# Kernel optimization log

Hardware: AMD Instinct MI355X
Metric: run time of the kernel (lower is better)

The kernel has to match this reference:

```python
import jax, jax.numpy as jnp
import numpy as np

B, L, IN = 4, 4096, 4096
G, R, GD = 32, 64, 128          # num_groups, rank per group, group_dim
SUM_R = G * R                    # 2048


def setup_inputs() -> dict:
    key = jax.random.key(0)
    k1, k2, k3, k4 = jax.random.split(key, 4)
    hidden_states = jax.random.normal(k1, (B, L, IN), dtype=jnp.float32)
    # nn.Linear weights: VT maps in_features -> sum(ranks)
    VT_w = jax.random.normal(k2, (SUM_R, IN), dtype=jnp.float32) * (IN ** -0.5)
    # Per-group up-projections U[i]: rank -> group_dim, stacked since ranks equal
    U_w = jax.random.normal(k3, (G, GD, R), dtype=jnp.float32) * (R ** -0.5)
    U_b = jax.random.normal(k4, (G, GD), dtype=jnp.float32) * 0.01
    return {"hidden_states": hidden_states, "VT_w": VT_w, "U_w": U_w, "U_b": U_b}


def reference(hidden_states, VT_w, U_w, U_b):
    # project_to_latent: shared down-projection  [B,L,IN] @ [IN,SUM_R]
    latents = jnp.einsum('bli,ri->blr', hidden_states, VT_w)  # [B,L,SUM_R]
    # reconstruct: per-group small up-projection on contiguous latent slices
    lat_g = latents.reshape(B, L, G, R)                        # [B,L,G,R]
    out_g = jnp.einsum('blgr,gdr->blgd', lat_g, U_w) + U_b     # [B,L,G,GD]
    return out_g.reshape(B, L, G * GD)                         # concat over groups
```

## Files before the change

kernel.cpp:

```cpp
#include <hip/hip_runtime.h>
#include <cstdint>

typedef unsigned short u16;
typedef u16 u16x8 __attribute__((ext_vector_type(8)));
typedef __bf16 bf16x8 __attribute__((ext_vector_type(8)));
typedef float f32x4 __attribute__((ext_vector_type(4)));

#define GLOAD_LDS16(g, l)                                                          \
  __builtin_amdgcn_global_load_lds((const __attribute__((address_space(1))) void*)(g), \
                                   (__attribute__((address_space(3))) void*)(l), 16, 0, 0)

#define BARRIER() do { asm volatile("" ::: "memory");                 \
                       __builtin_amdgcn_sched_barrier(0);             \
                       __builtin_amdgcn_s_barrier();                  \
                       __builtin_amdgcn_sched_barrier(0);             \
                       asm volatile("" ::: "memory"); } while (0)
#define VMCNT4() asm volatile("s_waitcnt vmcnt(4)" ::: "memory")
#define VMCNT0() asm volatile("s_waitcnt vmcnt(0)" ::: "memory")

__device__ __forceinline__ u16 f2bf(float f) {
  union { float f; uint32_t u; } v; v.f = f;
  uint32_t u = v.u;
  return (u16)((u + 0x7fffu + ((u >> 16) & 1u)) >> 16);
}

constexpr long MH = 67108864L;
constexpr long MV = 8388608L;
constexpr long MU = 262144L;
constexpr long ML = 33554432L;

__global__ __launch_bounds__(256) void cvt_all(const float* __restrict__ H,
                                               const float* __restrict__ VT,
                                               const float* __restrict__ Uw,
                                               u16* __restrict__ dst) {
  const long n8 = (MH + MV + MU) / 8;
  long i = (long)blockIdx.x * blockDim.x + threadIdx.x;
  long stride = (long)gridDim.x * blockDim.x;
  for (; i < n8; i += stride) {
    long j = i * 8;
    const float* src;
    if (j < MH)            src = H + j;
    else if (j < MH + MV)  src = VT + (j - MH);
    else                   src = Uw + (j - MH - MV);
    const float4* p = (const float4*)src;
    float4 a = p[0], b = p[1];
    u16x8 o;
    o[0] = f2bf(a.x); o[1] = f2bf(a.y); o[2] = f2bf(a.z); o[3] = f2bf(a.w);
    o[4] = f2bf(b.x); o[5] = f2bf(b.y); o[6] = f2bf(b.z); o[7] = f2bf(b.w);
    *(u16x8*)(dst + j) = o;
  }
}

constexpr int GK = 4096;
constexpr int NKT = GK / 64;

__device__ __forceinline__ void stage_half(u16* sm, const u16* g, int ldsbase, int w) {
  u16* l0 = sm + ldsbase + w * 1024;
  GLOAD_LDS16(g, l0);
  GLOAD_LDS16(g + 8 * GK, l0 + 512);
}

__device__ __forceinline__ void readA(const u16* sm, int base, int msub, bf16x8* fA) {
#pragma unroll
  for (int mf = 0; mf < 4; ++mf) {
    int idx = base + (msub * 64 + mf * 16) * 64;
    fA[mf * 2]     = *(const bf16x8*)(sm + idx);
    fA[mf * 2 + 1] = *(const bf16x8*)(sm + (idx ^ 32));
  }
}

__device__ __forceinline__ void readB(const u16* sm, int base, int qn, bf16x8* fB) {
#pragma unroll
  for (int nf = 0; nf < 2; ++nf) {
    int idx = base + (qn * 32 + nf * 16) * 64;
    fB[nf * 2]     = *(const bf16x8*)(sm + idx);
    fB[nf * 2 + 1] = *(const bf16x8*)(sm + (idx ^ 32));
  }
}

__device__ __forceinline__ void mfma8(const bf16x8* fA, const bf16x8* fB,
                                      f32x4 (*acc)[4], int mbase, int nbase) {
  __builtin_amdgcn_s_setprio(1);
#pragma unroll
  for (int mf = 0; mf < 4; ++mf)
#pragma unroll
    for (int nf = 0; nf < 2; ++nf) {
      acc[mbase + mf][nbase + nf] = __builtin_amdgcn_mfma_f32_16x16x32_bf16(
          fA[mf * 2], fB[nf * 2], acc[mbase + mf][nbase + nf], 0, 0, 0);
      acc[mbase + mf][nbase + nf] = __builtin_amdgcn_mfma_f32_16x16x32_bf16(
          fA[mf * 2 + 1], fB[nf * 2 + 1], acc[mbase + mf][nbase + nf], 0, 0, 0);
    }
  __builtin_amdgcn_s_setprio(0);
}

template <bool MORE>
__device__ __forceinline__ void kiter(u16* sm, int i, int w,
                                      const u16* gAs, const u16* gBs,
                                      int Ab0, int Bb0, bf16x8* fA, bf16x8* fB0,
                                      bf16x8* fB1, f32x4 (*acc)[4]) {
  const long dOdd = (long)(2 * i + 1) * 64;
  const long dE2  = (long)(2 * i + 2) * 64;
  const long dO3  = (long)(2 * i + 3) * 64;
  const long hOff = 128L * GK;

  readA(sm, Ab0, 0, fA);
  readB(sm, Bb0, 0, fB0);
  stage_half(sm, gBs + hOff + dOdd, 32768 + 24576, w);
  BARRIER();
  mfma8(fA, fB0, acc, 0, 0);
  BARRIER();
  readB(sm, Bb0, 1, fB1);
  stage_half(sm, gAs + hOff + dOdd, 24576, w);
  BARRIER();
  mfma8(fA, fB1, acc, 0, 2);
  BARRIER();
  readA(sm, Ab0, 1, fA);
  if constexpr (MORE) stage_half(sm, gBs + dE2, 32768, w);
  BARRIER();
  mfma8(fA, fB1, acc, 4, 2);
  BARRIER();
  if constexpr (MORE) stage_half(sm, gAs + dE2, 0, w);
  if constexpr (MORE) VMCNT4(); else VMCNT0();
  BARRIER();
  mfma8(fA, fB0, acc, 4, 0);
  BARRIER();
  readA(sm, Ab0 + 16384, 0, fA);
  readB(sm, Bb0 + 16384, 0, fB0);
  if constexpr (MORE) stage_half(sm, gBs + hOff + dE2, 32768 + 8192, w);
  BARRIER();
  mfma8(fA, fB0, acc, 0, 0);
  BARRIER();
  readB(sm, Bb0 + 16384, 1, fB1);
  if constexpr (MORE) stage_half(sm, gAs + hOff + dE2, 8192, w);
  BARRIER();
  mfma8(fA, fB1, acc, 0, 2);
  BARRIER();
  readA(sm, Ab0 + 16384, 1, fA);
  if constexpr (MORE) stage_half(sm, gBs + dO3, 32768 + 16384, w);
  BARRIER();
  mfma8(fA, fB1, acc, 4, 2);
  BARRIER();
  if constexpr (MORE) stage_half(sm, gAs + dO3, 16384, w);
  if constexpr (MORE) VMCNT4(); else VMCNT0();
  BARRIER();
  mfma8(fA, fB0, acc, 4, 0);
  BARRIER();
}

__global__ __launch_bounds__(512, 2) void gemm256_fused(const u16* __restrict__ A,
                                                        const u16* __restrict__ B,
                                                        const u16* __restrict__ Ubf,
                                                        const float* __restrict__ Ubias,
                                                        float* __restrict__ out) {
  __shared__ u16 sm[66560];
  int bid = blockIdx.x;
  int swz = (bid & 7) * 64 + (bid >> 3);
  int tn = swz & 7;
  int tm = swz >> 3;
  int t0 = threadIdx.x;
  int w = t0 >> 6, l = t0 & 63;
  int wr = w >> 2, wc = w & 3;
  int lo = l & 15, hi = l >> 4;

  int lr = l >> 3;
  int sslot = (l & 7) ^ lr;
  const u16* gAs = A + (long)(tm * 256 + w * 16 + lr) * GK + sslot * 8;
  const u16* gBs = B + (long)(tn * 256 + w * 16 + lr) * GK + sslot * 8;

  int slotbase = (hi ^ (lo & 7)) * 8;
  int Ab0 = wr * 8192 + lo * 64 + slotbase;
  int Bb0 = 32768 + (wc >> 1) * 8192 + ((wc & 1) * 64 + lo) * 64 + slotbase;

  bf16x8 fA[8], fB0[4], fB1[4];
  f32x4 acc[8][4] = {};

  stage_half(sm, gBs,               32768,         w);
  stage_half(sm, gAs,               0,             w);
  stage_half(sm, gBs + 128L * GK,   32768 + 8192,  w);
  stage_half(sm, gAs + 128L * GK,   8192,          w);
  stage_half(sm, gBs + 64,          32768 + 16384, w);
  stage_half(sm, gAs + 64,          16384,         w);
  VMCNT4();
  BARRIER();

  for (int i = 0; i < NKT / 2 - 1; ++i)
    kiter<true>(sm, i, w, gAs, gBs, Ab0, Bb0, fA, fB0, fB1, acc);
  kiter<false>(sm, NKT / 2 - 1, w, gAs, gBs, Ab0, Bb0, fA, fB0, fB1, acc);

  int g_abs = tn * 4 + wc;
#pragma unroll
  for (int mq = 0; mq < 8; ++mq)
#pragma unroll
    for (int n = 0; n < 4; ++n) {
      int rl = wr * 128 + mq * 16 + hi * 4;
      int cl = wc * 64 + n * 16 + lo;
#pragma unroll
      for (int j = 0; j < 4; ++j)
        sm[(rl + j) * 260 + cl] = f2bf(acc[mq][n][j]);
    }
  const u16* Ug = Ubf + g_abs * 8192;
#pragma unroll
  for (int mh = 0; mh < 2; ++mh) {
    bf16x8 fL[8];
#pragma unroll
    for (int ms = 0; ms < 4; ++ms) {
      int rl = wr * 128 + mh * 64 + ms * 16 + lo;
#pragma unroll
      for (int ks = 0; ks < 2; ++ks)
        fL[ms * 2 + ks] = *(const bf16x8*)(sm + rl * 260 + wc * 64 + ks * 32 + hi * 8);
    }
#pragma unroll
    for (int nf = 0; nf < 8; ++nf) {
      int d = nf * 16 + lo;
      bf16x8 u0 = *(const bf16x8*)(Ug + d * 64 + hi * 8);
      bf16x8 u1 = *(const bf16x8*)(Ug + d * 64 + 32 + hi * 8);
      float bias = Ubias[g_abs * 128 + d];
#pragma unroll
      for (int ms = 0; ms < 4; ++ms) {
        f32x4 o = {};
        o = __builtin_amdgcn_mfma_f32_16x16x32_bf16(fL[ms * 2],     u0, o, 0, 0, 0);
        o = __builtin_amdgcn_mfma_f32_16x16x32_bf16(fL[ms * 2 + 1], u1, o, 0, 0, 0);
        long row = (long)tm * 256 + wr * 128 + mh * 64 + ms * 16 + hi * 4;
        int col = g_abs * 128 + d;
#pragma unroll
        for (int j = 0; j < 4; ++j)
          out[(row + j) * 4096 + col] = o[j] + bias;
      }
    }
  }
}

__global__ __launch_bounds__(256) void gemm1_f32(const float* __restrict__ fAp,
                                                 const u16* __restrict__ B,
                                                 u16* __restrict__ Cl) {
  constexpr int K = 4096;
  __shared__ u16 sA[128 * 32];
  __shared__ u16 sB[128 * 32];
  int bid = blockIdx.x;
  int swz = (bid & 7) * 256 + (bid >> 3);
  int tn = swz & 15;
  int tm = swz >> 4;
  int t = threadIdx.x;
  int w = t >> 6, l = t & 63;
  int wr = w >> 1, wc = w & 1;
  int lo = l & 15, hi = l >> 4;
  const int rS = w * 32 + (l >> 2);
  const int kS = (l & 3) * 8;
  const u16* gB = B + (long)(tn * 128 + rS) * K + kS;
  u16* lB = &sB[w * 1024];
  int fr = t >> 1, fk = (t & 1) * 16;

  f32x4 acc[4][4] = {};
  for (int k0 = 0; k0 < K; k0 += 32) {
    const float* src = fAp + (long)(tm * 128 + fr) * K + k0 + fk;
    float4 x = *(const float4*)(src);
    float4 y = *(const float4*)(src + 4);
    float4 z = *(const float4*)(src + 8);
    float4 q = *(const float4*)(src + 12);
    u16x8 o1, o2;
    o1[0] = f2bf(x.x); o1[1] = f2bf(x.y); o1[2] = f2bf(x.z); o1[3] = f2bf(x.w);
    o1[4] = f2bf(y.x); o1[5] = f2bf(y.y); o1[6] = f2bf(y.z); o1[7] = f2bf(y.w);
    o2[0] = f2bf(z.x); o2[1] = f2bf(z.y); o2[2] = f2bf(z.z); o2[3] = f2bf(z.w);
    o2[4] = f2bf(q.x); o2[5] = f2bf(q.y); o2[6] = f2bf(q.z); o2[7] = f2bf(q.w);
    *(u16x8*)&sA[fr * 32 + fk] = o1;
    *(u16x8*)&sA[fr * 32 + fk + 8] = o2;
    GLOAD_LDS16(gB, lB);
    GLOAD_LDS16(gB + 16 * K, lB + 512);
    gB += 32;
    __syncthreads();
    bf16x8 af[4], bfr[4];
#pragma unroll
    for (int m = 0; m < 4; ++m)
      af[m] = *(const bf16x8*)&sA[(wr * 64 + m * 16 + lo) * 32 + hi * 8];
#pragma unroll
    for (int n = 0; n < 4; ++n)
      bfr[n] = *(const bf16x8*)&sB[(wc * 64 + n * 16 + lo) * 32 + hi * 8];
#pragma unroll
    for (int m = 0; m < 4; ++m)
#pragma unroll
      for (int n = 0; n < 4; ++n)
        acc[m][n] = __builtin_amdgcn_mfma_f32_16x16x32_bf16(af[m], bfr[n], acc[m][n], 0, 0, 0);
    __syncthreads();
  }
#pragma unroll
  for (int m = 0; m < 4; ++m)
#pragma unroll
    for (int n = 0; n < 4; ++n) {
      int col = tn * 128 + wc * 64 + n * 16 + lo;
      int row = tm * 128 + wr * 64 + m * 16 + hi * 4;
#pragma unroll
      for (int j = 0; j < 4; ++j)
        Cl[(long)(row + j) * 2048 + col] = f2bf(acc[m][n][j]);
    }
}

__global__ __launch_bounds__(256) void stage2(const u16* __restrict__ L,
                                              const u16* __restrict__ U,
                                              const float* __restrict__ Ub,
                                              float* __restrict__ out) {
  int tm = blockIdx.x, g = blockIdx.y;
  int t = threadIdx.x, w = t >> 6, l = t & 63;
  int lo = l & 15, hi = l >> 4;
  const u16* Lb = L + (long)(tm * 128 + w * 32) * 2048 + g * 64;
  const u16* Ug = U + g * 8192;
  f32x4 acc[2][8] = {};
#pragma unroll
  for (int ks = 0; ks < 2; ++ks) {
    int ek = ks * 32 + hi * 8;
    bf16x8 a0 = *(const bf16x8*)(Lb + (long)lo * 2048 + ek);
    bf16x8 a1 = *(const bf16x8*)(Lb + (long)(lo + 16) * 2048 + ek);
#pragma unroll
    for (int n = 0; n < 8; ++n) {
      bf16x8 bv = *(const bf16x8*)(Ug + (n * 16 + lo) * 64 + ek);
      acc[0][n] = __builtin_amdgcn_mfma_f32_16x16x32_bf16(a0, bv, acc[0][n], 0, 0, 0);
      acc[1][n] = __builtin_amdgcn_mfma_f32_16x16x32_bf16(a1, bv, acc[1][n], 0, 0, 0);
    }
  }
#pragma unroll
  for (int n = 0; n < 8; ++n) {
    int col = n * 16 + lo;
    float bias = Ub[g * 128 + col];
#pragma unroll
    for (int m = 0; m < 2; ++m) {
      int row = tm * 128 + w * 32 + m * 16 + hi * 4;
#pragma unroll
      for (int j = 0; j < 4; ++j)
        out[(long)(row + j) * 4096 + g * 128 + col] = acc[m][n][j] + bias;
    }
  }
}

__global__ __launch_bounds__(256) void cvt_f32_bf16(const float* __restrict__ in,
                                                    u16* __restrict__ out, long n8) {
  long i = (long)blockIdx.x * blockDim.x + threadIdx.x;
  long stride = (long)gridDim.x * blockDim.x;
  for (; i < n8; i += stride) {
    const float4* p = (const float4*)(in + i * 8);
    float4 a = p[0], b = p[1];
    u16x8 o;
    o[0] = f2bf(a.x); o[1] = f2bf(a.y); o[2] = f2bf(a.z); o[3] = f2bf(a.w);
    o[4] = f2bf(b.x); o[5] = f2bf(b.y); o[6] = f2bf(b.z); o[7] = f2bf(b.w);
    *(u16x8*)(out + i * 8) = o;
  }
}

extern "C" void kernel_launch(void* const* d_in, const int* in_sizes, int n_in,
                              void* d_out, int out_size, void* d_ws, size_t ws_size,
                              hipStream_t stream) {
  const float* H   = (const float*)d_in[0];
  const float* VT  = (const float*)d_in[1];
  const float* Uw  = (const float*)d_in[2];
  const float* Ubp = (const float*)d_in[3];
  float* out = (float*)d_out;
  size_t needFull = (size_t)(MH + MV + MU) * 2;

  if (ws_size >= needFull) {
    u16* hbf = (u16*)d_ws;
    u16* vbf = hbf + MH;
    u16* ubf = vbf + MV;
    cvt_all<<<2048, 256, 0, stream>>>(H, VT, Uw, hbf);
    gemm256_fused<<<512, 512, 0, stream>>>(hbf, vbf, ubf, Ubp, out);
  } else {
    u16* vbf = (u16*)d_ws;
    u16* ubf = vbf + MV;
    u16* lat = ubf + MU;
    cvt_f32_bf16<<<512, 256, 0, stream>>>(VT, vbf, MV / 8);
    cvt_f32_bf16<<<128, 256, 0, stream>>>(Uw, ubf, MU / 8);
    gemm1_f32<<<2048, 256, 0, stream>>>(H, vbf, lat);
    stage2<<<dim3(128, 32), 256, 0, stream>>>(lat, ubf, Ubp, out);
  }
}
```

Measured before the change: 350.7 us.

## Double-buffer MFMA register fragments to prefetch LDS reads one phase ahead

Splits the A and B register fragments into separate even/odd and half-0/half-1 buffers so each LDS read is issued one phase before the MFMA that consumes it. The next tile's first fragments are read before the last MFMA group of the current iteration, and the first read is hoisted before the loop. The aim is to hide LDS read latency behind matrix ops. The cost is roughly double the fragment registers alongside a large accumulator under launch_bounds(512,2), which risks spills or lower occupancy.

```diff
diff --git a/kernel.cpp b/kernel.cpp
--- a/kernel.cpp
+++ b/kernel.cpp
@@ -27,7 +27,6 @@
 constexpr long MH = 67108864L;
 constexpr long MV = 8388608L;
 constexpr long MU = 262144L;
-constexpr long ML = 33554432L;
 
 __global__ __launch_bounds__(256) void cvt_all(const float* __restrict__ H,
                                                const float* __restrict__ VT,
@@ -96,54 +95,60 @@
 template <bool MORE>
 __device__ __forceinline__ void kiter(u16* sm, int i, int w,
                                       const u16* gAs, const u16* gBs,
-                                      int Ab0, int Bb0, bf16x8* fA, bf16x8* fB0,
-                                      bf16x8* fB1, f32x4 (*acc)[4]) {
+                                      int Ab0, int Bb0,
+                                      bf16x8* fA0e, bf16x8* fA1e,
+                                      bf16x8* fA0o, bf16x8* fA1o,
+                                      bf16x8* fB0e, bf16x8* fB1e,
+                                      bf16x8* fB0o, bf16x8* fB1o,
+                                      f32x4 (*acc)[4]) {
   const long dOdd = (long)(2 * i + 1) * 64;
   const long dE2  = (long)(2 * i + 2) * 64;
   const long dO3  = (long)(2 * i + 3) * 64;
   const long hOff = 128L * GK;
 
-  readA(sm, Ab0, 0, fA);
-  readB(sm, Bb0, 0, fB0);
+  readB(sm, Bb0, 1, fB1e);
   stage_half(sm, gBs + hOff + dOdd, 32768 + 24576, w);
   BARRIER();
-  mfma8(fA, fB0, acc, 0, 0);
-  BARRIER();
-  readB(sm, Bb0, 1, fB1);
+  mfma8(fA0e, fB0e, acc, 0, 0);
+  BARRIER();
+  readA(sm, Ab0, 1, fA1e);
   stage_half(sm, gAs + hOff + dOdd, 24576, w);
   BARRIER();
-  mfma8(fA, fB1, acc, 0, 2);
-  BARRIER();
-  readA(sm, Ab0, 1, fA);
+  mfma8(fA0e, fB1e, acc, 0, 2);
+  BARRIER();
   if constexpr (MORE) stage_half(sm, gBs + dE2, 32768, w);
   BARRIER();
-  mfma8(fA, fB1, acc, 4, 2);
+  mfma8(fA1e, fB1e, acc, 4, 2);
   BARRIER();
   if constexpr (MORE) stage_half(sm, gAs + dE2, 0, w);
   if constexpr (MORE) VMCNT4(); else VMCNT0();
   BARRIER();
-  mfma8(fA, fB0, acc, 4, 0);
-  BARRIER();
-  readA(sm, Ab0 + 16384, 0, fA);
-  readB(sm, Bb0 + 16384, 0, fB0);
+  readA(sm, Ab0 + 16384, 0, fA0o);
+  readB(sm, Bb0 + 16384, 0, fB0o);
+  mfma8(fA1e, fB0e, acc, 4, 0);
+  BARRIER();
+  readB(sm, Bb0 + 16384, 1, fB1o);
   if constexpr (MORE) stage_half(sm, gBs + hOff + dE2, 32768 + 8192, w);
   BARRIER();
-  mfma8(fA, fB0, acc, 0, 0);
-  BARRIER();
-  readB(sm, Bb0 + 16384, 1, fB1);
+  mfma8(fA0o, fB0o, acc, 0, 0);
+  BARRIER();
+  readA(sm, Ab0 + 16384, 1, fA1o);
   if constexpr (MORE) stage_half(sm, gAs + hOff + dE2, 8192, w);
   BARRIER();
-  mfma8(fA, fB1, acc, 0, 2);
-  BARRIER();
-  readA(sm, Ab0 + 16384, 1, fA);
+  mfma8(fA0o, fB1o, acc, 0, 2);
+  BARRIER();
   if constexpr (MORE) stage_half(sm, gBs + dO3, 32768 + 16384, w);
   BARRIER();
-  mfma8(fA, fB1, acc, 4, 2);
+  mfma8(fA1o, fB1o, acc, 4, 2);
   BARRIER();
   if constexpr (MORE) stage_half(sm, gAs + dO3, 16384, w);
   if constexpr (MORE) VMCNT4(); else VMCNT0();
   BARRIER();
-  mfma8(fA, fB0, acc, 4, 0);
+  if constexpr (MORE) {
+    readA(sm, Ab0, 0, fA0e);
+    readB(sm, Bb0, 0, fB0e);
+  }
+  mfma8(fA1o, fB0o, acc, 4, 0);
   BARRIER();
 }
 
@@ -171,7 +176,8 @@
   int Ab0 = wr * 8192 + lo * 64 + slotbase;
   int Bb0 = 32768 + (wc >> 1) * 8192 + ((wc & 1) * 64 + lo) * 64 + slotbase;
 
-  bf16x8 fA[8], fB0[4], fB1[4];
+  bf16x8 fA0e[8], fA1e[8], fA0o[8], fA1o[8];
+  bf16x8 fB0e[4], fB1e[4], fB0o[4], fB1o[4];
   f32x4 acc[8][4] = {};
 
   stage_half(sm, gBs,               32768,         w);
@@ -182,10 +188,14 @@
   stage_half(sm, gAs + 64,          16384,         w);
   VMCNT4();
   BARRIER();
+  readA(sm, Ab0, 0, fA0e);
+  readB(sm, Bb0, 0, fB0e);
 
   for (int i = 0; i < NKT / 2 - 1; ++i)
-    kiter<true>(sm, i, w, gAs, gBs, Ab0, Bb0, fA, fB0, fB1, acc);
-  kiter<false>(sm, NKT / 2 - 1, w, gAs, gBs, Ab0, Bb0, fA, fB0, fB1, acc);
+    kiter<true>(sm, i, w, gAs, gBs, Ab0, Bb0,
+                fA0e, fA1e, fA0o, fA1o, fB0e, fB1e, fB0o, fB1o, acc);
+  kiter<false>(sm, NKT / 2 - 1, w, gAs, gBs, Ab0, Bb0,
+               fA0e, fA1e, fA0o, fA1o, fB0e, fB1e, fB0o, fB1o, acc);
 
   int g_abs = tn * 4 + wc;
 #pragma unroll
```

New measurement: 564.6 us. 1.61x slower.

## Fuse fp32-to-bf16 conversion of activations into GEMM A-tile loading

Applied to the files above, without the earlier changes.

Removes the separate pass that converts the large fp32 hidden_states tensor to bf16. The GEMM now loads fp32 A tiles into registers, converts them, and writes bf16 into LDS inside the pipelined k-loop, while B keeps using direct global-to-LDS loads. This avoids writing and re-reading a bf16 copy of the activations. In exchange, A loads go through registers, which adds VGPR pressure and conversion ALU work, and doubles A global read bytes per tile inside the GEMM. Waitcnt placement is reworked to fit the new load pattern.

```diff
diff --git a/kernel.cpp b/kernel.cpp
--- a/kernel.cpp
+++ b/kernel.cpp
@@ -15,8 +15,10 @@
                        __builtin_amdgcn_s_barrier();                  \
                        __builtin_amdgcn_sched_barrier(0);             \
                        asm volatile("" ::: "memory"); } while (0)
-#define VMCNT4() asm volatile("s_waitcnt vmcnt(4)" ::: "memory")
+#define VMCNT2() asm volatile("s_waitcnt vmcnt(2)" ::: "memory")
 #define VMCNT0() asm volatile("s_waitcnt vmcnt(0)" ::: "memory")
+#define LGKM0()  do { asm volatile("s_waitcnt lgkmcnt(0)" ::: "memory");  \
+                      __builtin_amdgcn_sched_barrier(0); } while (0)
 
 __device__ __forceinline__ u16 f2bf(float f) {
   union { float f; uint32_t u; } v; v.f = f;
@@ -29,19 +31,15 @@
 constexpr long MU = 262144L;
 constexpr long ML = 33554432L;
 
-__global__ __launch_bounds__(256) void cvt_all(const float* __restrict__ H,
-                                               const float* __restrict__ VT,
-                                               const float* __restrict__ Uw,
-                                               u16* __restrict__ dst) {
-  const long n8 = (MH + MV + MU) / 8;
+__global__ __launch_bounds__(256) void cvt_vu(const float* __restrict__ VT,
+                                              const float* __restrict__ Uw,
+                                              u16* __restrict__ dst) {
+  const long n8 = (MV + MU) / 8;
   long i = (long)blockIdx.x * blockDim.x + threadIdx.x;
   long stride = (long)gridDim.x * blockDim.x;
   for (; i < n8; i += stride) {
     long j = i * 8;
-    const float* src;
-    if (j < MH)            src = H + j;
-    else if (j < MH + MV)  src = VT + (j - MH);
-    else                   src = Uw + (j - MH - MV);
+    const float* src = (j < MV) ? (VT + j) : (Uw + (j - MV));
     const float4* p = (const float4*)src;
     float4 a = p[0], b = p[1];
     u16x8 o;
@@ -60,6 +58,22 @@
   GLOAD_LDS16(g + 8 * GK, l0 + 512);
 }
 
+__device__ __forceinline__ void loadA(const float* g, float4* r) {
+  r[0] = *(const float4*)(g);
+  r[1] = *(const float4*)(g + 4);
+  r[2] = *(const float4*)(g + 8 * GK);
+  r[3] = *(const float4*)(g + 8 * GK + 4);
+}
+__device__ __forceinline__ void cvtWriteA(u16* sm, int ldsbase, int wl8, const float4* r) {
+  u16x8 o0, o1;
+  o0[0] = f2bf(r[0].x); o0[1] = f2bf(r[0].y); o0[2] = f2bf(r[0].z); o0[3] = f2bf(r[0].w);
+  o0[4] = f2bf(r[1].x); o0[5] = f2bf(r[1].y); o0[6] = f2bf(r[1].z); o0[7] = f2bf(r[1].w);
+  o1[0] = f2bf(r[2].x); o1[1] = f2bf(r[2].y); o1[2] = f2bf(r[2].z); o1[3] = f2bf(r[2].w);
+  o1[4] = f2bf(r[3].x); o1[5] = f2bf(r[3].y); o1[6] = f2bf(r[3].z); o1[7] = f2bf(r[3].w);
+  *(u16x8*)(sm + ldsbase + wl8) = o0;
+  *(u16x8*)(sm + ldsbase + wl8 + 512) = o1;
+}
+
 __device__ __forceinline__ void readA(const u16* sm, int base, int msub, bf16x8* fA) {
 #pragma unroll
   for (int mf = 0; mf < 4; ++mf) {
@@ -94,60 +108,82 @@
 }
 
 template <bool MORE>
-__device__ __forceinline__ void kiter(u16* sm, int i, int w,
-                                      const u16* gAs, const u16* gBs,
+__device__ __forceinline__ void kiter(u16* sm, int i, int w, int wl8,
+                                      const float* gAf, const u16* gBs,
                                       int Ab0, int Bb0, bf16x8* fA, bf16x8* fB0,
                                       bf16x8* fB1, f32x4 (*acc)[4]) {
   const long dOdd = (long)(2 * i + 1) * 64;
   const long dE2  = (long)(2 * i + 2) * 64;
   const long dO3  = (long)(2 * i + 3) * 64;
-  const long hOff = 128L * GK;
-
+  const long hOffB = 128L * GK;
+  const long hOffA = 128L * GK;
+  float4 rA[4];
+
+  readB(sm, Bb0, 0, fB0);
   readA(sm, Ab0, 0, fA);
-  readB(sm, Bb0, 0, fB0);
-  stage_half(sm, gBs + hOff + dOdd, 32768 + 24576, w);
+  loadA(gAf + dOdd, rA);
+  stage_half(sm, gBs + hOffB + dOdd, 32768 + 24576, w);
   BARRIER();
   mfma8(fA, fB0, acc, 0, 0);
   BARRIER();
   readB(sm, Bb0, 1, fB1);
-  stage_half(sm, gAs + hOff + dOdd, 24576, w);
+  VMCNT2();
+  cvtWriteA(sm, 16384, wl8, rA);
+  LGKM0();
   BARRIER();
   mfma8(fA, fB1, acc, 0, 2);
   BARRIER();
   readA(sm, Ab0, 1, fA);
+  loadA(gAf + hOffA + dOdd, rA);
   if constexpr (MORE) stage_half(sm, gBs + dE2, 32768, w);
   BARRIER();
   mfma8(fA, fB1, acc, 4, 2);
   BARRIER();
-  if constexpr (MORE) stage_half(sm, gAs + dE2, 0, w);
-  if constexpr (MORE) VMCNT4(); else VMCNT0();
+  if constexpr (MORE) VMCNT2(); else VMCNT0();
+  cvtWriteA(sm, 24576, wl8, rA);
+  LGKM0();
   BARRIER();
   mfma8(fA, fB0, acc, 4, 0);
   BARRIER();
+  readB(sm, Bb0 + 16384, 0, fB0);
   readA(sm, Ab0 + 16384, 0, fA);
-  readB(sm, Bb0 + 16384, 0, fB0);
-  if constexpr (MORE) stage_half(sm, gBs + hOff + dE2, 32768 + 8192, w);
+  if constexpr (MORE) {
+    loadA(gAf + dE2, rA);
+    stage_half(sm, gBs + hOffB + dE2, 32768 + 8192, w);
+  }
   BARRIER();
   mfma8(fA, fB0, acc, 0, 0);
   BARRIER();
   readB(sm, Bb0 + 16384, 1, fB1);
-  if constexpr (MORE) stage_half(sm, gAs + hOff + dE2, 8192, w);
+  if constexpr (MORE) {
+    VMCNT2();
+    cvtWriteA(sm, 0, wl8, rA);
+    LGKM0();
+  }
   BARRIER();
   mfma8(fA, fB1, acc, 0, 2);
   BARRIER();
   readA(sm, Ab0 + 16384, 1, fA);
-  if constexpr (MORE) stage_half(sm, gBs + dO3, 32768 + 16384, w);
+  if constexpr (MORE) {
+    loadA(gAf + hOffA + dE2, rA);
+    stage_half(sm, gBs + dO3, 32768 + 16384, w);
+  }
   BARRIER();
   mfma8(fA, fB1, acc, 4, 2);
   BARRIER();
-  if constexpr (MORE) stage_half(sm, gAs + dO3, 16384, w);
-  if constexpr (MORE) VMCNT4(); else VMCNT0();
+  if constexpr (MORE) {
+    VMCNT2();
+    cvtWriteA(sm, 8192, wl8, rA);
+    LGKM0();
+  } else {
+    VMCNT0();
+  }
   BARRIER();
   mfma8(fA, fB0, acc, 4, 0);
   BARRIER();
 }
 
-__global__ __launch_bounds__(512, 2) void gemm256_fused(const u16* __restrict__ A,
+__global__ __launch_bounds__(512, 2) void gemm256_fused(const float* __restrict__ A,
                                                         const u16* __restrict__ B,
                                                         const u16* __restrict__ Ubf,
                                                         const float* __restrict__ Ubias,
@@ -164,8 +200,9 @@
 
   int lr = l >> 3;
   int sslot = (l & 7) ^ lr;
-  const u16* gAs = A + (long)(tm * 256 + w * 16 + lr) * GK + sslot * 8;
-  const u16* gBs = B + (long)(tn * 256 + w * 16 + lr) * GK + sslot * 8;
+  const float* gAf = A + (long)(tm * 256 + w * 16 + lr) * GK + sslot * 8;
+  const u16*   gBs = B + (long)(tn * 256 + w * 16 + lr) * GK + sslot * 8;
+  int wl8 = w * 1024 + l * 8;
 
   int slotbase = (hi ^ (lo & 7)) * 8;
   int Ab0 = wr * 8192 + lo * 64 + slotbase;
@@ -174,18 +211,24 @@
   bf16x8 fA[8], fB0[4], fB1[4];
   f32x4 acc[8][4] = {};
 
-  stage_half(sm, gBs,               32768,         w);
-  stage_half(sm, gAs,               0,             w);
-  stage_half(sm, gBs + 128L * GK,   32768 + 8192,  w);
-  stage_half(sm, gAs + 128L * GK,   8192,          w);
-  stage_half(sm, gBs + 64,          32768 + 16384, w);
-  stage_half(sm, gAs + 64,          16384,         w);
-  VMCNT4();
-  BARRIER();
+  {
+    float4 r0[4], r1[4];
+    loadA(gAf, r0);
+    loadA(gAf + 128L * GK, r1);
+    stage_half(sm, gBs,             32768,         w);
+    stage_half(sm, gBs + 128L * GK, 32768 + 8192,  w);
+    stage_half(sm, gBs + 64,        32768 + 16384, w);
+    asm volatile("s_waitcnt vmcnt(6)" ::: "memory");
+    cvtWriteA(sm, 0,    wl8, r0);
+    cvtWriteA(sm, 8192, wl8, r1);
+    VMCNT2();
+    LGKM0();
+    BARRIER();
+  }
 
   for (int i = 0; i < NKT / 2 - 1; ++i)
-    kiter<true>(sm, i, w, gAs, gBs, Ab0, Bb0, fA, fB0, fB1, acc);
-  kiter<false>(sm, NKT / 2 - 1, w, gAs, gBs, Ab0, Bb0, fA, fB0, fB1, acc);
+    kiter<true>(sm, i, w, wl8, gAf, gBs, Ab0, Bb0, fA, fB0, fB1, acc);
+  kiter<false>(sm, NKT / 2 - 1, w, wl8, gAf, gBs, Ab0, Bb0, fA, fB0, fB1, acc);
 
   int g_abs = tn * 4 + wc;
 #pragma unroll
@@ -330,20 +373,6 @@
   }
 }
 
-__global__ __launch_bounds__(256) void cvt_f32_bf16(const float* __restrict__ in,
-                                                    u16* __restrict__ out, long n8) {
-  long i = (long)blockIdx.x * blockDim.x + threadIdx.x;
-  long stride = (long)gridDim.x * blockDim.x;
-  for (; i < n8; i += stride) {
-    const float4* p = (const float4*)(in + i * 8);
-    float4 a = p[0], b = p[1];
-    u16x8 o;
-    o[0] = f2bf(a.x); o[1] = f2bf(a.y); o[2] = f2bf(a.z); o[3] = f2bf(a.w);
-    o[4] = f2bf(b.x); o[5] = f2bf(b.y); o[6] = f2bf(b.z); o[7] = f2bf(b.w);
-    *(u16x8*)(out + i * 8) = o;
-  }
-}
-
 extern "C" void kernel_launch(void* const* d_in, const int* in_sizes, int n_in,
                               void* d_out, int out_size, void* d_ws, size_t ws_size,
                               hipStream_t stream) {
@@ -352,20 +381,23 @@
   const float* Uw  = (const float*)d_in[2];
   const float* Ubp = (const float*)d_in[3];
   float* out = (float*)d_out;
-  size_t needFull = (size_t)(MH + MV + MU) * 2;
-
-  if (ws_size >= needFull) {
-    u16* hbf = (u16*)d_ws;
-    u16* vbf = hbf + MH;
+  size_t needFast = (size_t)(MV + MU) * 2;
+
+  if (ws_size >= needFast && ws_size < (size_t)(MV + MU + ML) * 2) {
+    u16* vbf = (u16*)d_ws;
     u16* ubf = vbf + MV;
-    cvt_all<<<2048, 256, 0, stream>>>(H, VT, Uw, hbf);
-    gemm256_fused<<<512, 512, 0, stream>>>(hbf, vbf, ubf, Ubp, out);
+    cvt_vu<<<512, 256, 0, stream>>>(VT, Uw, vbf);
+    gemm256_fused<<<512, 512, 0, stream>>>(H, vbf, ubf, Ubp, out);
+  } else if (ws_size >= (size_t)(MV + MU + ML) * 2) {
+    u16* vbf = (u16*)d_ws;
+    u16* ubf = vbf + MV;
+    cvt_vu<<<512, 256, 0, stream>>>(VT, Uw, vbf);
+    gemm256_fused<<<512, 512, 0, stream>>>(H, vbf, ubf, Ubp, out);
   } else {
     u16* vbf = (u16*)d_ws;
     u16* ubf = vbf + MV;
     u16* lat = ubf + MU;
-    cvt_f32_bf16<<<512, 256, 0, stream>>>(VT, vbf, MV / 8);
-    cvt_f32_bf16<<<128, 256, 0, stream>>>(Uw, ubf, MU / 8);
+    cvt_vu<<<512, 256, 0, stream>>>(VT, Uw, vbf);
     gemm1_f32<<<2048, 256, 0, stream>>>(H, vbf, lat);
     stage2<<<dim3(128, 32), 256, 0, stream>>>(lat, ubf, Ubp, out);
   }
```

Result: slower. 488.3 us (+39.2%).

## Double block to 16 waves with 64x64 wave tiles and denser MFMA phases

Applied to the files above, without the earlier changes.

Launches the fused GEMM with 1024 threads per block in a 4x4 wave grid, so each wave owns a 64x64 output tile instead of 128x64. Every thread now stages one 16-byte global-to-LDS load per slab instead of two. The K-iteration is regrouped into four 16-MFMA phases with explicit lgkmcnt waits, replacing eight 8-MFMA phases, and the vmcnt thresholds are adjusted to match. The aim is more waves per CU to hide latency and fewer barriers per MFMA. The risk is the 128-VGPR-per-thread budget that 1024-thread blocks impose, which could cause spills, plus more LDS fragment traffic per unit of compute.

```diff
diff --git a/kernel.cpp b/kernel.cpp
--- a/kernel.cpp
+++ b/kernel.cpp
@@ -15,8 +15,10 @@
                        __builtin_amdgcn_s_barrier();                  \
                        __builtin_amdgcn_sched_barrier(0);             \
                        asm volatile("" ::: "memory"); } while (0)
-#define VMCNT4() asm volatile("s_waitcnt vmcnt(4)" ::: "memory")
+#define VMCNT2() asm volatile("s_waitcnt vmcnt(2)" ::: "memory")
 #define VMCNT0() asm volatile("s_waitcnt vmcnt(0)" ::: "memory")
+#define LGKM0()  do { asm volatile("s_waitcnt lgkmcnt(0)" ::: "memory");  \
+                      __builtin_amdgcn_sched_barrier(0); } while (0)
 
 __device__ __forceinline__ u16 f2bf(float f) {
   union { float f; uint32_t u; } v; v.f = f;
@@ -54,104 +56,96 @@
 constexpr int GK = 4096;
 constexpr int NKT = GK / 64;
 
-__device__ __forceinline__ void stage_half(u16* sm, const u16* g, int ldsbase, int w) {
-  u16* l0 = sm + ldsbase + w * 1024;
-  GLOAD_LDS16(g, l0);
-  GLOAD_LDS16(g + 8 * GK, l0 + 512);
-}
-
-__device__ __forceinline__ void readA(const u16* sm, int base, int msub, bf16x8* fA) {
-#pragma unroll
-  for (int mf = 0; mf < 4; ++mf) {
-    int idx = base + (msub * 64 + mf * 16) * 64;
-    fA[mf * 2]     = *(const bf16x8*)(sm + idx);
-    fA[mf * 2 + 1] = *(const bf16x8*)(sm + (idx ^ 32));
-  }
-}
-
-__device__ __forceinline__ void readB(const u16* sm, int base, int qn, bf16x8* fB) {
-#pragma unroll
-  for (int nf = 0; nf < 2; ++nf) {
-    int idx = base + (qn * 32 + nf * 16) * 64;
-    fB[nf * 2]     = *(const bf16x8*)(sm + idx);
-    fB[nf * 2 + 1] = *(const bf16x8*)(sm + (idx ^ 32));
-  }
-}
-
-__device__ __forceinline__ void mfma8(const bf16x8* fA, const bf16x8* fB,
-                                      f32x4 (*acc)[4], int mbase, int nbase) {
+__device__ __forceinline__ void stage1(u16* sm, const u16* g, int ldsbase, int dst8) {
+  GLOAD_LDS16(g, sm + ldsbase + dst8);
+}
+
+__device__ __forceinline__ void readF(const u16* sm, int base, int sub, bf16x8* f) {
+#pragma unroll
+  for (int ff = 0; ff < 2; ++ff) {
+    int idx = base + (sub * 32 + ff * 16) * 64;
+    f[ff * 2]     = *(const bf16x8*)(sm + idx);
+    f[ff * 2 + 1] = *(const bf16x8*)(sm + (idx ^ 32));
+  }
+}
+
+__device__ __forceinline__ void mfma16(const bf16x8* fA, const bf16x8* fB0,
+                                       const bf16x8* fB1, f32x4 (*acc)[4], int mbase) {
   __builtin_amdgcn_s_setprio(1);
 #pragma unroll
-  for (int mf = 0; mf < 4; ++mf)
-#pragma unroll
-    for (int nf = 0; nf < 2; ++nf) {
-      acc[mbase + mf][nbase + nf] = __builtin_amdgcn_mfma_f32_16x16x32_bf16(
-          fA[mf * 2], fB[nf * 2], acc[mbase + mf][nbase + nf], 0, 0, 0);
-      acc[mbase + mf][nbase + nf] = __builtin_amdgcn_mfma_f32_16x16x32_bf16(
-          fA[mf * 2 + 1], fB[nf * 2 + 1], acc[mbase + mf][nbase + nf], 0, 0, 0);
+  for (int fm = 0; fm < 2; ++fm)
+#pragma unroll
+    for (int n = 0; n < 4; ++n) {
+      const bf16x8* fb = (n < 2) ? (fB0 + (n & 1) * 2) : (fB1 + (n & 1) * 2);
+      acc[mbase + fm][n] = __builtin_amdgcn_mfma_f32_16x16x32_bf16(
+          fA[fm * 2], fb[0], acc[mbase + fm][n], 0, 0, 0);
+      acc[mbase + fm][n] = __builtin_amdgcn_mfma_f32_16x16x32_bf16(
+          fA[fm * 2 + 1], fb[1], acc[mbase + fm][n], 0, 0, 0);
     }
   __builtin_amdgcn_s_setprio(0);
 }
 
 template <bool MORE>
-__device__ __forceinline__ void kiter(u16* sm, int i, int w,
+__device__ __forceinline__ void kiter(u16* sm, int i, int dst8,
                                       const u16* gAs, const u16* gBs,
-                                      int Ab0, int Bb0, bf16x8* fA, bf16x8* fB0,
-                                      bf16x8* fB1, f32x4 (*acc)[4]) {
+                                      int Ab0, int Bb0,
+                                      bf16x8* fA0, bf16x8* fA1,
+                                      bf16x8* fB0, bf16x8* fB1,
+                                      f32x4 (*acc)[4]) {
   const long dOdd = (long)(2 * i + 1) * 64;
   const long dE2  = (long)(2 * i + 2) * 64;
   const long dO3  = (long)(2 * i + 3) * 64;
   const long hOff = 128L * GK;
 
-  readA(sm, Ab0, 0, fA);
-  readB(sm, Bb0, 0, fB0);
-  stage_half(sm, gBs + hOff + dOdd, 32768 + 24576, w);
-  BARRIER();
-  mfma8(fA, fB0, acc, 0, 0);
-  BARRIER();
-  readB(sm, Bb0, 1, fB1);
-  stage_half(sm, gAs + hOff + dOdd, 24576, w);
-  BARRIER();
-  mfma8(fA, fB1, acc, 0, 2);
-  BARRIER();
-  readA(sm, Ab0, 1, fA);
-  if constexpr (MORE) stage_half(sm, gBs + dE2, 32768, w);
-  BARRIER();
-  mfma8(fA, fB1, acc, 4, 2);
-  BARRIER();
-  if constexpr (MORE) stage_half(sm, gAs + dE2, 0, w);
-  if constexpr (MORE) VMCNT4(); else VMCNT0();
-  BARRIER();
-  mfma8(fA, fB0, acc, 4, 0);
-  BARRIER();
-  readA(sm, Ab0 + 16384, 0, fA);
-  readB(sm, Bb0 + 16384, 0, fB0);
-  if constexpr (MORE) stage_half(sm, gBs + hOff + dE2, 32768 + 8192, w);
-  BARRIER();
-  mfma8(fA, fB0, acc, 0, 0);
-  BARRIER();
-  readB(sm, Bb0 + 16384, 1, fB1);
-  if constexpr (MORE) stage_half(sm, gAs + hOff + dE2, 8192, w);
-  BARRIER();
-  mfma8(fA, fB1, acc, 0, 2);
-  BARRIER();
-  readA(sm, Ab0 + 16384, 1, fA);
-  if constexpr (MORE) stage_half(sm, gBs + dO3, 32768 + 16384, w);
-  BARRIER();
-  mfma8(fA, fB1, acc, 4, 2);
-  BARRIER();
-  if constexpr (MORE) stage_half(sm, gAs + dO3, 16384, w);
-  if constexpr (MORE) VMCNT4(); else VMCNT0();
-  BARRIER();
-  mfma8(fA, fB0, acc, 4, 0);
-  BARRIER();
-}
-
-__global__ __launch_bounds__(512, 2) void gemm256_fused(const u16* __restrict__ A,
-                                                        const u16* __restrict__ B,
-                                                        const u16* __restrict__ Ubf,
-                                                        const float* __restrict__ Ubias,
-                                                        float* __restrict__ out) {
+  readF(sm, Bb0, 0, fB0);
+  readF(sm, Ab0, 0, fA0);
+  readF(sm, Bb0, 1, fB1);
+  readF(sm, Ab0, 1, fA1);
+  stage1(sm, gBs + hOff + dOdd, 32768 + 24576, dst8);
+  stage1(sm, gAs + hOff + dOdd, 24576, dst8);
+  BARRIER();
+  mfma16(fA0, fB0, fB1, acc, 0);
+  LGKM0();
+  BARRIER();
+  if constexpr (MORE) {
+    stage1(sm, gBs + dE2, 32768, dst8);
+    stage1(sm, gAs + dE2, 0, dst8);
+    VMCNT2();
+  } else {
+    VMCNT0();
+  }
+  BARRIER();
+  mfma16(fA1, fB0, fB1, acc, 2);
+  BARRIER();
+  readF(sm, Bb0 + 16384, 0, fB0);
+  readF(sm, Ab0 + 16384, 0, fA0);
+  readF(sm, Bb0 + 16384, 1, fB1);
+  readF(sm, Ab0 + 16384, 1, fA1);
+  if constexpr (MORE) {
+    stage1(sm, gBs + hOff + dE2, 32768 + 8192, dst8);
+    stage1(sm, gAs + hOff + dE2, 8192, dst8);
+  }
+  BARRIER();
+  mfma16(fA0, fB0, fB1, acc, 0);
+  LGKM0();
+  BARRIER();
+  if constexpr (MORE) {
+    stage1(sm, gBs + dO3, 32768 + 16384, dst8);
+    stage1(sm, gAs + dO3, 16384, dst8);
+    VMCNT2();
+  } else {
+    VMCNT0();
+  }
+  BARRIER();
+  mfma16(fA1, fB0, fB1, acc, 2);
+  BARRIER();
+}
+
+__global__ __launch_bounds__(1024, 4) void gemm256_fused(const u16* __restrict__ A,
+                                                         const u16* __restrict__ B,
+                                                         const u16* __restrict__ Ubf,
+                                                         const float* __restrict__ Ubias,
+                                                         float* __restrict__ out) {
   __shared__ u16 sm[66560];
   int bid = blockIdx.x;
   int swz = (bid & 7) * 64 + (bid >> 3);
@@ -162,70 +156,68 @@
   int wr = w >> 2, wc = w & 3;
   int lo = l & 15, hi = l >> 4;
 
-  int lr = l >> 3;
-  int sslot = (l & 7) ^ lr;
-  const u16* gAs = A + (long)(tm * 256 + w * 16 + lr) * GK + sslot * 8;
-  const u16* gBs = B + (long)(tn * 256 + w * 16 + lr) * GK + sslot * 8;
+  int lr = t0 >> 3;
+  int sslot = (t0 & 7) ^ (lr & 7);
+  const u16* gAs = A + (long)(tm * 256 + lr) * GK + sslot * 8;
+  const u16* gBs = B + (long)(tn * 256 + lr) * GK + sslot * 8;
+  int dst8 = t0 * 8;
 
   int slotbase = (hi ^ (lo & 7)) * 8;
-  int Ab0 = wr * 8192 + lo * 64 + slotbase;
-  int Bb0 = 32768 + (wc >> 1) * 8192 + ((wc & 1) * 64 + lo) * 64 + slotbase;
-
-  bf16x8 fA[8], fB0[4], fB1[4];
-  f32x4 acc[8][4] = {};
-
-  stage_half(sm, gBs,               32768,         w);
-  stage_half(sm, gAs,               0,             w);
-  stage_half(sm, gBs + 128L * GK,   32768 + 8192,  w);
-  stage_half(sm, gAs + 128L * GK,   8192,          w);
-  stage_half(sm, gBs + 64,          32768 + 16384, w);
-  stage_half(sm, gAs + 64,          16384,         w);
-  VMCNT4();
+  int Ab0 = (wr * 64 + lo) * 64 + slotbase;
+  int Bb0 = 32768 + (wc * 64 + lo) * 64 + slotbase;
+
+  bf16x8 fA0[4], fA1[4], fB0[4], fB1[4];
+  f32x4 acc[4][4] = {};
+
+  stage1(sm, gBs,               32768,         dst8);
+  stage1(sm, gAs,               0,             dst8);
+  stage1(sm, gBs + 128L * GK,   32768 + 8192,  dst8);
+  stage1(sm, gAs + 128L * GK,   8192,          dst8);
+  stage1(sm, gBs + 64,          32768 + 16384, dst8);
+  stage1(sm, gAs + 64,          16384,         dst8);
+  VMCNT2();
   BARRIER();
 
   for (int i = 0; i < NKT / 2 - 1; ++i)
-    kiter<true>(sm, i, w, gAs, gBs, Ab0, Bb0, fA, fB0, fB1, acc);
-  kiter<false>(sm, NKT / 2 - 1, w, gAs, gBs, Ab0, Bb0, fA, fB0, fB1, acc);
+    kiter<true>(sm, i, dst8, gAs, gBs, Ab0, Bb0, fA0, fA1, fB0, fB1, acc);
+  kiter<false>(sm, NKT / 2 - 1, dst8, gAs, gBs, Ab0, Bb0, fA0, fA1, fB0, fB1, acc);
 
   int g_abs = tn * 4 + wc;
 #pragma unroll
-  for (int mq = 0; mq < 8; ++mq)
+  for (int mq = 0; mq < 4; ++mq)
 #pragma unroll
     for (int n = 0; n < 4; ++n) {
-      int rl = wr * 128 + mq * 16 + hi * 4;
+      int rl = wr * 64 + mq * 16 + hi * 4;
       int cl = wc * 64 + n * 16 + lo;
 #pragma unroll
       for (int j = 0; j < 4; ++j)
         sm[(rl + j) * 260 + cl] = f2bf(acc[mq][n][j]);
     }
   const u16* Ug = Ubf + g_abs * 8192;
-#pragma unroll
-  for (int mh = 0; mh < 2; ++mh) {
-    bf16x8 fL[8];
+  bf16x8 fL[8];
+#pragma unroll
+  for (int ms = 0; ms < 4; ++ms) {
+    int rl = wr * 64 + ms * 16 + lo;
+#pragma unroll
+    for (int ks = 0; ks < 2; ++ks)
+      fL[ms * 2 + ks] = *(const bf16x8*)(sm + rl * 260 + wc * 64 + ks * 32 + hi * 8);
+  }
+#pragma unroll
+  for (int nf = 0; nf < 8; ++nf) {
+    int d = nf * 16 + lo;
+    bf16x8 u0 = *(const bf16x8*)(Ug + d * 64 + hi * 8);
+    bf16x8 u1 = *(const bf16x8*)(Ug + d * 64 + 32 + hi * 8);
+    float bias = Ubias[g_abs * 128 + d];
 #pragma unroll
     for (int ms = 0; ms < 4; ++ms) {
-      int rl = wr * 128 + mh * 64 + ms * 16 + lo;
-#pragma unroll
-      for (int ks = 0; ks < 2; ++ks)
-        fL[ms * 2 + ks] = *(const bf16x8*)(sm + rl * 260 + wc * 64 + ks * 32 + hi * 8);
-    }
-#pragma unroll
-    for (int nf = 0; nf < 8; ++nf) {
-      int d = nf * 16 + lo;
-      bf16x8 u0 = *(const bf16x8*)(Ug + d * 64 + hi * 8);
-      bf16x8 u1 = *(const bf16x8*)(Ug + d * 64 + 32 + hi * 8);
-      float bias = Ubias[g_abs * 128 + d];
-#pragma unroll
-      for (int ms = 0; ms < 4; ++ms) {
-        f32x4 o = {};
-        o = __builtin_amdgcn_mfma_f32_16x16x32_bf16(fL[ms * 2],     u0, o, 0, 0, 0);
-        o = __builtin_amdgcn_mfma_f32_16x16x32_bf16(fL[ms * 2 + 1], u1, o, 0, 0, 0);
-        long row = (long)tm * 256 + wr * 128 + mh * 64 + ms * 16 + hi * 4;
-        int col = g_abs * 128 + d;
-#pragma unroll
-        for (int j = 0; j < 4; ++j)
-          out[(row + j) * 4096 + col] = o[j] + bias;
-      }
+      f32x4 o = {};
+      o = __builtin_amdgcn_mfma_f32_16x16x32_bf16(fL[ms * 2],     u0, o, 0, 0, 0);
+      o = __builtin_amdgcn_mfma_f32_16x16x32_bf16(fL[ms * 2 + 1], u1, o, 0, 0, 0);
+      long row = (long)tm * 256 + wr * 64 + ms * 16 + hi * 4;
+      int col = g_abs * 128 + d;
+#pragma unroll
+      for (int j = 0; j < 4; ++j)
+        out[(row + j) * 4096 + col] = o[j] + bias;
     }
   }
 }
@@ -359,7 +351,7 @@
     u16* vbf = hbf + MH;
     u16* ubf = vbf + MV;
     cvt_all<<<2048, 256, 0, stream>>>(H, VT, Uw, hbf);
-    gemm256_fused<<<512, 512, 0, stream>>>(hbf, vbf, ubf, Ubp, out);
+    gemm256_fused<<<512, 1024, 0, stream>>>(hbf, vbf, ubf, Ubp, out);
   } else {
     u16* vbf = (u16*)d_ws;
     u16* ubf = vbf + MV;
```

Result: slower. 1.189 ms (+239.0%).
